# Optimization experiments

Measured on AMD Instinct MI355X. Metric: run time of the kernel, lower is better.

The kernel has to match this reference:

```python
import jax, jax.numpy as jnp
import numpy as np

B, C, H, W = 4, 256, 64, 64
DQK = C // 4


def setup_inputs() -> dict:
    key = jax.random.key(0)
    ks = jax.random.split(key, 5)
    s = 0.05
    x = jax.random.normal(ks[0], (B, C, H, W), dtype=jnp.float32)
    Wq = jax.random.normal(ks[1], (DQK, C), dtype=jnp.float32) * s
    Wk = jax.random.normal(ks[2], (DQK, C), dtype=jnp.float32) * s
    Wv = jax.random.normal(ks[3], (C, C), dtype=jnp.float32) * s
    bq = jnp.zeros((DQK,), jnp.float32)
    bk = jnp.zeros((DQK,), jnp.float32)
    bv = jnp.zeros((C,), jnp.float32)
    gamma = jnp.zeros((1,), jnp.float32)
    return {"x": x, "Wq": Wq, "bq": bq, "Wk": Wk, "bk": bk,
            "Wv": Wv, "bv": bv, "gamma": gamma}


def reference(x, Wq, bq, Wk, bk, Wv, bv, gamma):
    b, c, h, w = x.shape
    n = h * w
    xf = x.reshape(b, c, n)                      # [B, C, N]
    # 1x1 convs == per-pixel linear projections
    q = jnp.einsum('dc,bcn->bnd', Wq, xf) + bq   # [B, N, Dqk]
    k = jnp.einsum('dc,bcn->bdn', Wk, xf) + bk[None, :, None]  # [B, Dqk, N]
    v = jnp.einsum('ec,bcn->ben', Wv, xf) + bv[None, :, None]  # [B, C, N]
    energy = jnp.einsum('bnd,bdm->bnm', q, k)    # [B, N, N]
    attn = jax.nn.softmax(energy, axis=-1)       # softmax over keys
    # out[b,c,i] = sum_j v[b,c,j] * attn[b,i,j]
    out = jnp.einsum('bcj,bij->bci', v, attn)    # [B, C, N]
    out = out.reshape(b, c, h, w)
    return gamma * out + x
```

## Files before the change

### kernel.cpp

```cpp
#include <hip/hip_runtime.h>

#define B_ 4
#define C_ 256
#define N_ 4096
#define D_ 64

typedef __bf16 bf16x8 __attribute__((ext_vector_type(8)));
typedef float floatx4 __attribute__((ext_vector_type(4)));
typedef float floatx16 __attribute__((ext_vector_type(16)));
typedef unsigned short ushort8v __attribute__((ext_vector_type(8)));
typedef unsigned short ushort4v __attribute__((ext_vector_type(4)));
typedef unsigned short ushort2v __attribute__((ext_vector_type(2)));

static __device__ __forceinline__ unsigned short f2bf(float f) {
    unsigned int u = __builtin_bit_cast(unsigned int, f);
    u += 0x7fffu + ((u >> 16) & 1u);
    return (unsigned short)(u >> 16);
}
static __device__ __forceinline__ float bf2f(unsigned short h) {
    unsigned int u = ((unsigned int)h) << 16;
    return __builtin_bit_cast(float, u);
}
static __device__ __forceinline__ unsigned int cvt_pk_bf16(float lo, float hi) {
    unsigned int d;
    asm("v_cvt_pk_bf16_f32 %0, %1, %2" : "=v"(d) : "v"(lo), "v"(hi));
    return d;
}

#define GLOAD16(gp, lp)                                                      \
    __builtin_amdgcn_global_load_lds(                                        \
        (const __attribute__((address_space(1))) void*)(gp),                 \
        (__attribute__((address_space(3))) void*)(lp), 16, 0, 0)

__global__ __launch_bounds__(256) void convert_w(
    const float* __restrict__ Wq, const float* __restrict__ Wk,
    const float* __restrict__ Wv, unsigned short* __restrict__ WbfA)
{
    int tid = blockIdx.x * 256 + threadIdx.x;
    int p0  = tid * 4;
    int j0   = p0 & 7;
    int lane = (p0 >> 3) & 63;
    int sidx = p0 >> 9;
    int ft = sidx >> 3, ks = sidx & 7;
    int m  = lane & 15, g = lane >> 4;
    int f  = 16*ft + m;
    int c  = 32*ks + 8*g + j0;
    const float* src = (f < 64)  ? (Wq + (size_t)f * C_)
                     : (f < 128) ? (Wk + (size_t)(f - 64) * C_)
                                 : (Wv + (size_t)(f - 128) * C_);
    float4 v = *(const float4*)(src + c);
    uint2 u;
    u.x = cvt_pk_bf16(v.x, v.y);
    u.y = cvt_pk_bf16(v.z, v.w);
    *(uint2*)(WbfA + p0) = u;
}

__global__ __launch_bounds__(256, 4) void proj_kernel(
    const float* __restrict__ x, const unsigned short* __restrict__ WbfA,
    const float* __restrict__ bq, const float* __restrict__ bk,
    const float* __restrict__ bv,
    unsigned short* __restrict__ Qg, unsigned short* __restrict__ Kg,
    unsigned short* __restrict__ Vg)
{
    __shared__ __align__(16) unsigned short smem[64 * 264];
    unsigned short* xs = smem;
    unsigned short* Lt = smem;

    const int n0 = blockIdx.x * 64;
    const int f0 = blockIdx.y * 128;
    const int b  = blockIdx.z;
    const int t  = threadIdx.x;
    const int w  = t >> 6;
    const int lane = t & 63;
    const int g  = lane >> 4;
    const int m  = lane & 15;

#pragma unroll
    for (int k = 0; k < 8; ++k) {
        int e  = t + 256 * k;
        int cp = e >> 4;
        int c  = 2 * cp;
        int n4 = (e & 15) * 4;
        float4 v0 = *(const float4*)(x + ((size_t)b*C_ + c    )*N_ + n0 + n4);
        float4 v1 = *(const float4*)(x + ((size_t)b*C_ + c + 1)*N_ + n0 + n4);
        float a0[4] = {v0.x, v0.y, v0.z, v0.w};
        float a1[4] = {v1.x, v1.y, v1.z, v1.w};
#pragma unroll
        for (int j = 0; j < 4; ++j) {
            int n = n4 + j;
            unsigned int u = cvt_pk_bf16(a0[j], a1[j]);
            *(unsigned int*)&xs[n*264 + (((c >> 3) ^ (n & 7)) << 3) + (c & 7)] = u;
        }
    }

    float bias_[2][4];
#pragma unroll
    for (int mt = 0; mt < 2; ++mt)
#pragma unroll
        for (int r = 0; r < 4; ++r) {
            int fg = f0 + 32*w + 16*mt + 4*g + r;
            bias_[mt][r] = (fg < 64) ? bq[fg]
                         : (fg < 128) ? bk[fg - 64] : bv[fg - 128];
        }

    const unsigned short* Wa0 = WbfA + (size_t)(((f0 >> 4) + 2*w    )*8)*512
                              + lane*8;
    const unsigned short* Wa1 = WbfA + (size_t)(((f0 >> 4) + 2*w + 1)*8)*512
                              + lane*8;

    floatx4 acc[2][4];
#pragma unroll
    for (int mt = 0; mt < 2; ++mt)
#pragma unroll
        for (int nt = 0; nt < 4; ++nt) acc[mt][nt] = (floatx4){0.f,0.f,0.f,0.f};

    __syncthreads();

#pragma unroll
    for (int ks = 0; ks < 8; ++ks) {
        bf16x8 af[2];
        af[0] = *(const bf16x8*)(Wa0 + ks*512);
        af[1] = *(const bf16x8*)(Wa1 + ks*512);
#pragma unroll
        for (int nt = 0; nt < 4; ++nt) {
            int n = 16*nt + m;
            bf16x8 bfr = *(const bf16x8*)
                &xs[n*264 + (((4*ks + g) ^ (n & 7)) << 3)];
#pragma unroll
            for (int mt = 0; mt < 2; ++mt)
                acc[mt][nt] = __builtin_amdgcn_mfma_f32_16x16x32_bf16(
                                  af[mt], bfr, acc[mt][nt], 0, 0, 0);
        }
    }

    __syncthreads();

#pragma unroll
    for (int mt = 0; mt < 2; ++mt)
#pragma unroll
        for (int nt = 0; nt < 4; ++nt)
#pragma unroll
            for (int r = 0; r < 4; ++r)
                Lt[(32*w + 16*mt + 4*g + r)*72 + 16*nt + m] =
                    f2bf(acc[mt][nt][r] + bias_[mt][r]);
    __syncthreads();

    if (f0 == 0) {
        const int fq0 = (t >> 4) * 8;
        const int nl4 = (t & 15) * 4;
        ushort4v col[8];
#pragma unroll
        for (int j = 0; j < 8; ++j)
            col[j] = *(const ushort4v*)&Lt[(fq0 + j)*72 + nl4];
#pragma unroll
        for (int c = 0; c < 4; ++c) {
            ushort8v u;
#pragma unroll
            for (int j = 0; j < 8; ++j) u[j] = col[j][c];
            int nl = nl4 + c;
            unsigned short* dst = (fq0 < 64)
                ? (Qg + ((size_t)b*N_ + n0 + nl)*D_ + fq0)
                : (Kg + ((size_t)b*N_ + n0 + nl)*D_ + (fq0 - 64));
            *(ushort8v*)dst = u;
        }
    } else {
        const int cb = f0 - 128;
#pragma unroll
        for (int k = 0; k < 4; ++k) {
            int e  = t + 256 * k;
            int fr = e >> 3;
            int n8 = (e & 7) * 8;
            ushort8v u = *(const ushort8v*)&Lt[fr*72 + n8];
            *(ushort8v*)(Vg + ((size_t)b*C_ + cb + fr)*N_ + n0 + n8) = u;
        }
    }
}

__global__ __launch_bounds__(512, 2) void flash_kernel(
    const unsigned short* __restrict__ Qg, const unsigned short* __restrict__ Kg,
    const unsigned short* __restrict__ Vg,
    unsigned short* __restrict__ Opart, float* __restrict__ ML)
{
    __shared__ __align__(16) unsigned short Vlds[3][32 * 512];
    __shared__ __align__(16) unsigned short Klds[2][8 * 512];
    __shared__ float AL[8][32];

    const int gx   = blockIdx.x;
    const int tile = blockIdx.y;
    const int quarter = gx & 3;
    const int b    = gx >> 2;
    const int n0   = tile * 256;
    const int t    = threadIdx.x;
    const int w    = t >> 6;
    const int lane = t & 63;
    const int q32  = lane & 31;
    const int h    = lane >> 5;

    const unsigned short* Qb = Qg + ((size_t)b*N_ + n0)*D_;
    const unsigned short* Kb = Kg + (size_t)b*N_*D_;
    const unsigned short* Vb = Vg + (size_t)b*C_*N_;

    const int cstart = quarter * 16;
    const int cend   = cstart + 16;

    bf16x8 qf[4];
#pragma unroll
    for (int ks = 0; ks < 4; ++ks)
        qf[ks] = *(const bf16x8*)(Qb + (size_t)(32*w + q32)*D_ + 16*ks + 8*h);

    floatx16 accO[8];
#pragma unroll
    for (int ct = 0; ct < 8; ++ct)
#pragma unroll
        for (int r = 0; r < 16; ++r) accO[ct][r] = 0.f;

    float mrow = -1e30f, lrow = 0.f;
    bf16x8 pa_prev[4];
    bool skip_prev = true;

#define STAGE_K(T64, BUF) do {                                               \
    const unsigned short* gp = Kb                                            \
        + (size_t)((T64)*64 + 32*(w >> 2) + q32)*D_ + 16*(w & 3) + 8*h;      \
    GLOAD16(gp, &Klds[BUF][w * 512]); } while (0)

#define STAGE_V(T64, BUF) do {                                               \
    _Pragma("unroll")                                                        \
    for (int u_ = 0; u_ < 4; ++u_) {                                         \
        const unsigned short* gp = Vb                                        \
            + (size_t)(32*w + q32)*N_ + (T64)*64 + 16*u_ + 8*h;              \
        GLOAD16(gp, &Vlds[BUF][(w*4 + u_) * 512]);                           \
    } } while (0)

#define FITER(T64, HASPV, HASPRE) do {                                       \
    if (HASPRE) { STAGE_K((T64)+1, kcur ^ 1); STAGE_V((T64)+1, vnxt); }      \
                                                          \
    floatx16 accS[2];                                                        \
    _Pragma("unroll")                                                        \
    for (int kt = 0; kt < 2; ++kt)                                           \
        _Pragma("unroll")                                                    \
        for (int r = 0; r < 16; ++r) accS[kt][r] = 0.f;                      \
    _Pragma("unroll")                                                        \
    for (int kt = 0; kt < 2; ++kt)                                           \
        _Pragma("unroll")                                                    \
        for (int ks = 0; ks < 4; ++ks) {                                     \
            bf16x8 kfr = *(const bf16x8*)                                    \
                &Klds[kcur][(kt*4 + ks)*512 + lane*8];                       \
            accS[kt] = __builtin_amdgcn_mfma_f32_32x32x16_bf16(              \
                           kfr, qf[ks], accS[kt], 0, 0, 0);                  \
        }                                                                    \
                 \
    if (HASPV) {                                                             \
        if (!skip_prev) {                                                    \
            float4 av_[4];                                                   \
            _Pragma("unroll")                                                \
            for (int gp_ = 0; gp_ < 4; ++gp_)                                \
                av_[gp_] = *(const float4*)&AL[w][8*gp_ + 4*h];              \
            _Pragma("unroll")                                                \
            for (int ct = 0; ct < 8; ++ct)                                   \
                _Pragma("unroll")                                            \
                for (int gp_ = 0; gp_ < 4; ++gp_)                            \
                    _Pragma("unroll")                                        \
                    for (int i_ = 0; i_ < 4; ++i_)                           \
                        accO[ct][4*gp_ + i_] *= av_[gp_][i_];                \
        }                                                                    \
        __builtin_amdgcn_s_setprio(1);                                       \
        _Pragma("unroll")                                                    \
        for (int ct = 0; ct < 8; ++ct)                                       \
            _Pragma("unroll")                                                \
            for (int kc = 0; kc < 4; ++kc) {                                 \
                bf16x8 vf = *(const bf16x8*)                                 \
                    &Vlds[vprv][(ct*4 + kc)*512 + lane*8];                   \
                accO[ct] = __builtin_amdgcn_mfma_f32_32x32x16_bf16(          \
                               pa_prev[kc], vf, accO[ct], 0, 0, 0);          \
            }                                                                \
        __builtin_amdgcn_s_setprio(0);                                       \
    }                                                                        \
                               \
    float mx = -1e30f;                                                       \
    _Pragma("unroll")                                                        \
    for (int kt = 0; kt < 2; ++kt)                                           \
        _Pragma("unroll")                                                    \
        for (int r = 0; r < 16; ++r) mx = fmaxf(mx, accS[kt][r]);            \
    mx = fmaxf(mx, __shfl_xor(mx, 32));                                      \
    bool skip = __all(mx <= mrow + 8.f) != 0;                                \
    float mnew  = skip ? mrow : fmaxf(mrow, mx);                             \
    float alpha = __expf(mrow - mnew);                                       \
    mrow = mnew;                                                             \
    float p_[2][16];                                                         \
    float rs = 0.f;                                                          \
    _Pragma("unroll")                                                        \
    for (int kt = 0; kt < 2; ++kt)                                           \
        _Pragma("unroll")                                                    \
        for (int r = 0; r < 16; ++r) {                                       \
            float e_ = __expf(accS[kt][r] - mnew);                           \
            p_[kt][r] = e_;                                                  \
            rs += e_;                                                        \
        }                                                                    \
    rs += __shfl_xor(rs, 32);                                                \
    lrow = lrow * alpha + rs;                                                \
    if (!skip && h == 0) AL[w][q32] = alpha;                                 \
    skip_prev = skip;                                                        \
                      \
    _Pragma("unroll")                                                        \
    for (int kt = 0; kt < 2; ++kt)                                           \
        _Pragma("unroll")                                                    \
        for (int cp = 0; cp < 2; ++cp) {                                     \
            unsigned int Y0 = cvt_pk_bf16(p_[kt][8*cp + 0], p_[kt][8*cp + 1]);\
            unsigned int Y1 = cvt_pk_bf16(p_[kt][8*cp + 2], p_[kt][8*cp + 3]);\
            unsigned int X0 = cvt_pk_bf16(p_[kt][8*cp + 4], p_[kt][8*cp + 5]);\
            unsigned int X1 = cvt_pk_bf16(p_[kt][8*cp + 6], p_[kt][8*cp + 7]);\
            asm volatile("v_permlane32_swap_b32 %0, %1" : "+v"(Y0), "+v"(X0));\
            asm volatile("v_permlane32_swap_b32 %0, %1" : "+v"(Y1), "+v"(X1));\
            uint4 fu; fu.x = Y0; fu.y = Y1; fu.z = X0; fu.w = X1;            \
            pa_prev[kt*2 + cp] = __builtin_bit_cast(bf16x8, fu);             \
        }                                                                    \
    __syncthreads();        \
    vprv = vcur; vcur = vnxt; vnxt = (vnxt + 1 == 3) ? 0 : vnxt + 1;         \
    kcur ^= 1;                                                               \
} while (0)

    STAGE_K(cstart, 0);
    STAGE_V(cstart, 0);
    __syncthreads();

    int vcur = 0, vnxt = 1, vprv = 2, kcur = 0;

    FITER(cstart, 0, 1);
    for (int t64 = cstart + 1; t64 < cend - 1; ++t64)
        FITER(t64, 1, 1);
    FITER(cend - 1, 1, 0);

    if (!skip_prev) {
        float4 av_[4];
#pragma unroll
        for (int gp_ = 0; gp_ < 4; ++gp_)
            av_[gp_] = *(const float4*)&AL[w][8*gp_ + 4*h];
#pragma unroll
        for (int ct = 0; ct < 8; ++ct)
#pragma unroll
            for (int gp_ = 0; gp_ < 4; ++gp_)
#pragma unroll
                for (int i_ = 0; i_ < 4; ++i_)
                    accO[ct][4*gp_ + i_] *= av_[gp_][i_];
    }
#pragma unroll
    for (int ct = 0; ct < 8; ++ct)
#pragma unroll
        for (int kc = 0; kc < 4; ++kc) {
            bf16x8 vf = *(const bf16x8*)
                &Vlds[vprv][(ct*4 + kc)*512 + lane*8];
            accO[ct] = __builtin_amdgcn_mfma_f32_32x32x16_bf16(
                           pa_prev[kc], vf, accO[ct], 0, 0, 0);
        }

    const size_t tbase = ((size_t)(quarter*B_ + b)*16 + tile);
    unsigned short* Ob = Opart + tbase * (C_ * 256);
    float* ml = ML + tbase * 512;

    if (h == 0) {
        ml[32*w + q32]       = mrow;
        ml[256 + 32*w + q32] = lrow;
    }

#pragma unroll
    for (int ct = 0; ct < 8; ++ct) {
        int c = 32*ct + q32;
#pragma unroll
        for (int gp = 0; gp < 4; ++gp) {
            uint2 pu;
            pu.x = cvt_pk_bf16(accO[ct][4*gp + 0], accO[ct][4*gp + 1]);
            pu.y = cvt_pk_bf16(accO[ct][4*gp + 2], accO[ct][4*gp + 3]);
            *(uint2*)(Ob + (size_t)c*256 + 32*w + 8*gp + 4*h) = pu;
        }
    }
#undef FITER
#undef STAGE_K
#undef STAGE_V
}

__global__ __launch_bounds__(256) void combine_kernel(
    const unsigned short* __restrict__ Opart, const float* __restrict__ ML,
    const float* __restrict__ x, const float* __restrict__ gamma,
    float* __restrict__ out)
{
    __shared__ float sc[4][256];
    const int tile   = blockIdx.x;
    const int cslice = blockIdx.y;
    const int b      = blockIdx.z;
    const int n0     = tile * 256;
    const int t      = threadIdx.x;

    {
        float mm[4], ll[4];
        float M = -1e30f;
#pragma unroll
        for (int s = 0; s < 4; ++s) {
            const float* mls = ML + ((size_t)(s*B_ + b)*16 + tile)*512;
            mm[s] = mls[t];
            ll[s] = mls[256 + t];
            M = fmaxf(M, mm[s]);
        }
        float fs[4];
        float L = 0.f;
#pragma unroll
        for (int s = 0; s < 4; ++s) { fs[s] = __expf(mm[s] - M); L += fs[s]*ll[s]; }
        float gm = gamma[0];
#pragma unroll
        for (int s = 0; s < 4; ++s) sc[s][t] = gm * fs[s] / L;
    }
    __syncthreads();

    const int nq = t & 63;
    const int cl = t >> 6;
    const float* xb = x   + (size_t)b*C_*N_;
    float*       ob = out + (size_t)b*C_*N_;
    const unsigned short* Os[4];
#pragma unroll
    for (int s = 0; s < 4; ++s)
        Os[s] = Opart + ((size_t)(s*B_ + b)*16 + tile)*(C_*256);

    float sv[4][4];
#pragma unroll
    for (int s = 0; s < 4; ++s)
#pragma unroll
        for (int k = 0; k < 4; ++k) sv[s][k] = sc[s][4*nq + k];

#pragma unroll
    for (int i = 0; i < 8; ++i) {
        int c = 32*cslice + 4*i + cl;
        float4 x4 = *(const float4*)(xb + (size_t)c*N_ + n0 + 4*nq);
        float4 y = x4;
#pragma unroll
        for (int s = 0; s < 4; ++s) {
            ushort4v a4 = *(const ushort4v*)(Os[s] + (size_t)c*256 + 4*nq);
            y.x += sv[s][0]*bf2f(a4[0]);
            y.y += sv[s][1]*bf2f(a4[1]);
            y.z += sv[s][2]*bf2f(a4[2]);
            y.w += sv[s][3]*bf2f(a4[3]);
        }
        *(float4*)(ob + (size_t)c*N_ + n0 + 4*nq) = y;
    }
}

extern "C" void kernel_launch(void* const* d_in, const int* in_sizes, int n_in,
                              void* d_out, int out_size, void* d_ws, size_t ws_size,
                              hipStream_t stream) {
    const float* x     = (const float*)d_in[0];
    const float* Wq    = (const float*)d_in[1];
    const float* bq    = (const float*)d_in[2];
    const float* Wk    = (const float*)d_in[3];
    const float* bk    = (const float*)d_in[4];
    const float* Wv    = (const float*)d_in[5];
    const float* bv    = (const float*)d_in[6];
    const float* gamma = (const float*)d_in[7];
    float* out = (float*)d_out;

    unsigned short* Qg = (unsigned short*)d_ws;
    unsigned short* Kg = Qg + (size_t)B_*N_*D_;
    unsigned short* Vg = Kg + (size_t)B_*N_*D_;
    unsigned short* Op = Vg + (size_t)B_*C_*N_;
    float* ML = (float*)(Op + (size_t)4*B_*16*C_*256);
    unsigned short* WbfA = (unsigned short*)(ML + (size_t)4*B_*16*512);

    convert_w<<<dim3(96), 256, 0, stream>>>(Wq, Wk, Wv, WbfA);
    proj_kernel<<<dim3(64, 3, 4), 256, 0, stream>>>(x, WbfA, bq, bk, bv,
                                                    Qg, Kg, Vg);
    flash_kernel<<<dim3(16, 16), 512, 0, stream>>>(Qg, Kg, Vg, Op, ML);
    combine_kernel<<<dim3(16, 8, 4), 256, 0, stream>>>(Op, ML, x, gamma, out);
}
```

Baseline: 162.3 us.

## Pre-transpose x to bf16 once and merge weight conversion into that kernel

Adds a kernel that converts x to bf16 and transposes it to a pixel-major layout, and the same kernel also does the weight conversion that used to run as its own launch. The projection kernel now loads that transposed bf16 tile straight into LDS with global_load_lds in MFMA fragment order. Before, each of the three feature-block groups read and converted the fp32 x tile separately, so x was read three times and the conversion was repeated. In exchange there is an extra bf16 round trip through global memory for Xt and a dependency between two launches.

```diff
diff --git a/kernel.cpp b/kernel.cpp
--- a/kernel.cpp
+++ b/kernel.cpp
@@ -32,48 +32,38 @@
         (const __attribute__((address_space(1))) void*)(gp),                 \
         (__attribute__((address_space(3))) void*)(lp), 16, 0, 0)
 
-__global__ __launch_bounds__(256) void convert_w(
+__global__ __launch_bounds__(256, 4) void xtw_kernel(
+    const float* __restrict__ x,
     const float* __restrict__ Wq, const float* __restrict__ Wk,
-    const float* __restrict__ Wv, unsigned short* __restrict__ WbfA)
+    const float* __restrict__ Wv,
+    unsigned short* __restrict__ WbfA, unsigned short* __restrict__ Xt)
 {
-    int tid = blockIdx.x * 256 + threadIdx.x;
-    int p0  = tid * 4;
-    int j0   = p0 & 7;
-    int lane = (p0 >> 3) & 63;
-    int sidx = p0 >> 9;
-    int ft = sidx >> 3, ks = sidx & 7;
-    int m  = lane & 15, g = lane >> 4;
-    int f  = 16*ft + m;
-    int c  = 32*ks + 8*g + j0;
-    const float* src = (f < 64)  ? (Wq + (size_t)f * C_)
-                     : (f < 128) ? (Wk + (size_t)(f - 64) * C_)
-                                 : (Wv + (size_t)(f - 128) * C_);
-    float4 v = *(const float4*)(src + c);
-    uint2 u;
-    u.x = cvt_pk_bf16(v.x, v.y);
-    u.y = cvt_pk_bf16(v.z, v.w);
-    *(uint2*)(WbfA + p0) = u;
-}
-
-__global__ __launch_bounds__(256, 4) void proj_kernel(
-    const float* __restrict__ x, const unsigned short* __restrict__ WbfA,
-    const float* __restrict__ bq, const float* __restrict__ bk,
-    const float* __restrict__ bv,
-    unsigned short* __restrict__ Qg, unsigned short* __restrict__ Kg,
-    unsigned short* __restrict__ Vg)
-{
-    __shared__ __align__(16) unsigned short smem[64 * 264];
-    unsigned short* xs = smem;
-    unsigned short* Lt = smem;
+    __shared__ __align__(16) unsigned short xs[64 * 264];
 
     const int n0 = blockIdx.x * 64;
-    const int f0 = blockIdx.y * 128;
-    const int b  = blockIdx.z;
+    const int b  = blockIdx.y;
     const int t  = threadIdx.x;
-    const int w  = t >> 6;
-    const int lane = t & 63;
-    const int g  = lane >> 4;
-    const int m  = lane & 15;
+    const int gid = blockIdx.x + 64 * blockIdx.y;
+
+    if (gid < 96) {
+        int tid = gid * 256 + t;
+        int p0  = tid * 4;
+        int j0   = p0 & 7;
+        int lane = (p0 >> 3) & 63;
+        int sidx = p0 >> 9;
+        int ft = sidx >> 3, ks = sidx & 7;
+        int m  = lane & 15, g = lane >> 4;
+        int f  = 16*ft + m;
+        int c  = 32*ks + 8*g + j0;
+        const float* src = (f < 64)  ? (Wq + (size_t)f * C_)
+                         : (f < 128) ? (Wk + (size_t)(f - 64) * C_)
+                                     : (Wv + (size_t)(f - 128) * C_);
+        float4 v = *(const float4*)(src + c);
+        uint2 u;
+        u.x = cvt_pk_bf16(v.x, v.y);
+        u.y = cvt_pk_bf16(v.z, v.w);
+        *(uint2*)(WbfA + p0) = u;
+    }
 
 #pragma unroll
     for (int k = 0; k < 8; ++k) {
@@ -92,6 +82,42 @@
             *(unsigned int*)&xs[n*264 + (((c >> 3) ^ (n & 7)) << 3) + (c & 7)] = u;
         }
     }
+    __syncthreads();
+
+#pragma unroll
+    for (int pass = 0; pass < 8; ++pass) {
+        int n  = 8*pass + (t >> 5);
+        int cc = t & 31;
+        ushort8v v = *(const ushort8v*)&xs[n*264 + ((cc ^ (n & 7)) << 3)];
+        *(ushort8v*)(Xt + ((size_t)b*N_ + n0 + n)*256 + 8*cc) = v;
+    }
+}
+
+__global__ __launch_bounds__(256, 4) void proj_kernel(
+    const unsigned short* __restrict__ Xt, const unsigned short* __restrict__ WbfA,
+    const float* __restrict__ bq, const float* __restrict__ bk,
+    const float* __restrict__ bv,
+    unsigned short* __restrict__ Qg, unsigned short* __restrict__ Kg,
+    unsigned short* __restrict__ Vg)
+{
+    __shared__ __align__(16) unsigned short xslds[32 * 512];
+    unsigned short* Lt = xslds;
+
+    const int n0 = blockIdx.x * 64;
+    const int f0 = blockIdx.y * 128;
+    const int b  = blockIdx.z;
+    const int t  = threadIdx.x;
+    const int w  = t >> 6;
+    const int lane = t & 63;
+    const int g  = lane >> 4;
+    const int m  = lane & 15;
+
+#pragma unroll
+    for (int u = 0; u < 8; ++u) {
+        const unsigned short* gp = Xt
+            + ((size_t)b*N_ + n0 + 16*w + m)*256 + 32*u + 8*g;
+        GLOAD16(gp, &xslds[(w*8 + u) * 512]);
+    }
 
     float bias_[2][4];
 #pragma unroll
@@ -123,9 +149,7 @@
         af[1] = *(const bf16x8*)(Wa1 + ks*512);
 #pragma unroll
         for (int nt = 0; nt < 4; ++nt) {
-            int n = 16*nt + m;
-            bf16x8 bfr = *(const bf16x8*)
-                &xs[n*264 + (((4*ks + g) ^ (n & 7)) << 3)];
+            bf16x8 bfr = *(const bf16x8*)&xslds[(nt*8 + ks)*512 + lane*8];
 #pragma unroll
             for (int mt = 0; mt < 2; ++mt)
                 acc[mt][nt] = __builtin_amdgcn_mfma_f32_16x16x32_bf16(
@@ -461,9 +485,10 @@
     unsigned short* Op = Vg + (size_t)B_*C_*N_;
     float* ML = (float*)(Op + (size_t)4*B_*16*C_*256);
     unsigned short* WbfA = (unsigned short*)(ML + (size_t)4*B_*16*512);
-
-    convert_w<<<dim3(96), 256, 0, stream>>>(Wq, Wk, Wv, WbfA);
-    proj_kernel<<<dim3(64, 3, 4), 256, 0, stream>>>(x, WbfA, bq, bk, bv,
+    unsigned short* Xt = WbfA + (size_t)98304;
+
+    xtw_kernel<<<dim3(64, 4), 256, 0, stream>>>(x, Wq, Wk, Wv, WbfA, Xt);
+    proj_kernel<<<dim3(64, 3, 4), 256, 0, stream>>>(Xt, WbfA, bq, bk, bv,
                                                     Qg, Kg, Vg);
     flash_kernel<<<dim3(16, 16), 512, 0, stream>>>(Qg, Kg, Vg, Op, ML);
     combine_kernel<<<dim3(16, 8, 4), 256, 0, stream>>>(Op, ML, x, gamma, out);
```

Result: no change. 163.9 us (+1.0%).
